# Kernel optimization log

Measured on AMD Instinct MI355X. Metric: run time of the kernel, lower is better.

Reference implementation:

```python
import jax, jax.numpy as jnp
import numpy as np

def setup_inputs() -> dict:
    key = jax.random.key(0)
    k1, k2, k3, k4 = jax.random.split(key, 4)
    B, S, IN, OUT = 4, 2048, 4096, 11008
    x = jax.random.normal(k1, (B, S, IN), dtype=jnp.float32)
    int8_weight = jax.random.randint(k2, (OUT, IN), -128, 128, dtype=jnp.int32)
    scale = jax.random.uniform(k3, (1,), dtype=jnp.float32) * 0.01 + 1e-4
    bias = jax.random.normal(k4, (OUT,), dtype=jnp.float32)
    return {"x": x, "int8_weight": int8_weight, "scale": scale, "bias": bias}

def reference(x, int8_weight, scale, bias):
    # dequantize int8 weight with per-tensor scale, then linear: y = x @ W^T + b
    weight = int8_weight.astype(jnp.float32) * scale[0]  # [OUT, IN]
    return jnp.einsum('bsi,oi->bso', x, weight) + bias
```

## Files before the change

kernel.cpp:

```cpp
#include <hip/hip_runtime.h>
#include <stdint.h>

typedef __attribute__((ext_vector_type(4))) int   int4v;
typedef __attribute__((ext_vector_type(4))) float f32x4;

#define K_DIM 4096
#define N_DIM 11008
#define M_DIM 8192
#define BM 256
#define BN 256
#define BKB 128
#define NT (K_DIM / BKB)
#define MT2 (M_DIM / BM)
#define NT2 (N_DIM / BN)

__global__ __launch_bounds__(256) void quant_x_kernel(
    const float* __restrict__ x, unsigned char* __restrict__ xq,
    float* __restrict__ srow)
{
    const int row = blockIdx.x;
    const float4* xr = (const float4*)(x + (size_t)row * K_DIM);
    float4 v[4];
    float m = 0.f;
    #pragma unroll
    for (int i = 0; i < 4; ++i) {
        v[i] = xr[threadIdx.x + 256 * i];
        m = fmaxf(m, fmaxf(fmaxf(fabsf(v[i].x), fabsf(v[i].y)),
                           fmaxf(fabsf(v[i].z), fabsf(v[i].w))));
    }
    #pragma unroll
    for (int off = 32; off; off >>= 1) m = fmaxf(m, __shfl_xor(m, off, 64));
    __shared__ float wmax[4];
    if ((threadIdx.x & 63) == 0) wmax[threadIdx.x >> 6] = m;
    __syncthreads();
    const float mb  = fmaxf(fmaxf(wmax[0], wmax[1]), fmaxf(wmax[2], wmax[3]));
    const float s   = (mb > 0.f) ? mb * (1.f / 127.f) : 1.f;
    const float inv = (mb > 0.f) ? 127.f / mb : 0.f;
    if (threadIdx.x == 0) srow[row] = s;
    uint32_t* oq = (uint32_t*)(xq + (size_t)row * K_DIM);
    #pragma unroll
    for (int i = 0; i < 4; ++i) {
        int a = __float2int_rn(v[i].x * inv), b = __float2int_rn(v[i].y * inv);
        int c = __float2int_rn(v[i].z * inv), d = __float2int_rn(v[i].w * inv);
        oq[threadIdx.x + 256 * i] =
            (a & 0xff) | ((b & 0xff) << 8) | ((c & 0xff) << 16) | ((d & 0xff) << 24);
    }
}

__global__ void cvt_w8_kernel(const int* __restrict__ w,
                              uint2* __restrict__ wq, int n8) {
    int i = blockIdx.x * blockDim.x + threadIdx.x;
    if (i >= n8) return;
    const int4* p = (const int4*)w + 2 * (size_t)i;
    int4 a = p[0], b = p[1];
    uint32_t lo = (a.x & 0xff) | ((a.y & 0xff) << 8) | ((a.z & 0xff) << 16) | ((a.w & 0xff) << 24);
    uint32_t hi = (b.x & 0xff) | ((b.y & 0xff) << 8) | ((b.z & 0xff) << 16) | ((b.w & 0xff) << 24);
    wq[i] = (uint2){lo, hi};
}

#define GLDS16(gsrc, ldst)                                                       \
    __builtin_amdgcn_global_load_lds(                                            \
        (const __attribute__((address_space(1))) void*)(gsrc),                   \
        (__attribute__((address_space(3))) void*)(ldst), 16, 0, 0)

#define BARSCHED() do { __builtin_amdgcn_s_barrier();                            \
                        __builtin_amdgcn_sched_barrier(0); } while (0)
#define VMCNT(n)  asm volatile("s_waitcnt vmcnt(" #n ")" ::: "memory")

__global__ __launch_bounds__(512, 2) void gemm2_kernel(
    const unsigned char* __restrict__ xq,
    const unsigned char* __restrict__ wq,
    const float* __restrict__ srow,
    const float* __restrict__ scale,
    const float* __restrict__ bias,
    float* __restrict__ out)
{
    __shared__ unsigned char sm[131072];
    char* smc = (char*)sm;

    const int T  = threadIdx.x;
    const int l  = T & 63;
    const int wv = T >> 6;
    const int wm = wv >> 2;
    const int wn = wv & 3;

    const int orig = blockIdx.x;
    const int xcd  = orig & 7;
    const int p    = orig >> 3;
    const int bm   = xcd * 4 + (p & 3);
    const int bn   = p >> 2;
    const size_t rowM0 = (size_t)bm * BM;
    const size_t rowN0 = (size_t)bn * BN;

    const int rowT = T >> 3;
    const int colT = (((T & 7) * 16) ^ ((rowT & 7) << 4));
    const unsigned char* pAg = xq + (rowM0 + rowT) * (size_t)K_DIM + colT;
    const unsigned char* pBg = wq + (rowN0 + ((rowT >> 5) << 6) + (rowT & 31)) * (size_t)K_DIM + colT;

    auto stageA = [&](char* base, int Q, int kt) {
        #pragma unroll
        for (int c = 0; c < 2; ++c) {
            const unsigned char* src = pAg + (size_t)(c * 128 + Q * 64) * K_DIM + (size_t)kt * BKB;
            char* dst = base + Q * 16384 + c * 8192 + T * 16;
            GLDS16(src, dst);
        }
    };
    auto stageB = [&](char* base, int Q, int kt) {
        #pragma unroll
        for (int c = 0; c < 2; ++c) {
            const unsigned char* src = pBg + (size_t)(c * 128 + Q * 32) * K_DIM + (size_t)kt * BKB;
            char* dst = base + 32768 + Q * 16384 + c * 8192 + T * 16;
            GLDS16(src, dst);
        }
    };

    const int sw     = (l & 7) << 4;
    const int inrow0 = (l >> 4) * 16;
    const int lowk0  = inrow0 ^ sw;
    const int lowk1  = (64 + inrow0) ^ sw;
    const int arow   = wm * 64 + (l & 15);
    const int brow   = wn * 32 + (l & 15);

    int4v acc[8][4];
    #pragma unroll
    for (int i = 0; i < 8; ++i)
        #pragma unroll
        for (int j = 0; j < 4; ++j)
            acc[i][j] = (int4v){0, 0, 0, 0};

    int4v Ah[4][2];
    int4v Bh[4][2];

    char* const b0 = smc;
    char* const b1 = smc + 65536;

#define READ_A(base)                                                             \
    _Pragma("unroll")                                                            \
    for (int im = 0; im < 4; ++im) {                                             \
        Ah[im][0] = *(const int4v*)((base) + (arow + im * 16) * 128 + lowk0);    \
        Ah[im][1] = *(const int4v*)((base) + (arow + im * 16) * 128 + lowk1);    \
    }
#define READ_B(base, f0)                                                         \
    _Pragma("unroll")                                                            \
    for (int f = 0; f < 2; ++f) {                                                \
        Bh[(f0) + f][0] = *(const int4v*)((base) + (brow + f * 16) * 128 + lowk0); \
        Bh[(f0) + f][1] = *(const int4v*)((base) + (brow + f * 16) * 128 + lowk1); \
    }
#define MFMAQ(mi, ni)                                                            \
    __builtin_amdgcn_s_setprio(1);                                               \
    _Pragma("unroll")                                                            \
    for (int im = 0; im < 4; ++im)                                               \
        _Pragma("unroll")                                                        \
        for (int jn = 0; jn < 2; ++jn)                                           \
            _Pragma("unroll")                                                    \
            for (int kk = 0; kk < 2; ++kk)                                       \
                acc[(mi) + im][(ni) + jn] = __builtin_amdgcn_mfma_i32_16x16x64_i8( \
                    Ah[im][kk], Bh[(ni) + jn][kk], acc[(mi) + im][(ni) + jn], 0, 0, 0); \
    __builtin_amdgcn_s_setprio(0);

#define TILE_BODY(bcur, bnxt, EE, ST0, STN, RD)                                  \
    READ_B((bcur) + 32768 + 16384, 2);                                           \
    if (ST0) stageA((bnxt), 1, (EE) + 1);                                        \
    BARSCHED();                                                                  \
    MFMAQ(0, 0);                                                                 \
    __builtin_amdgcn_sched_barrier(0);                                           \
    if (STN) stageA((bcur), 0, (EE) + 2);                                        \
    BARSCHED();                                                                  \
    MFMAQ(0, 2);                                                                 \
    READ_A((bcur) + 16384);                                                      \
    __builtin_amdgcn_sched_barrier(0);                                           \
    if (STN) stageB((bcur), 0, (EE) + 2);                                        \
    BARSCHED();                                                                  \
    MFMAQ(4, 0);                                                                 \
    if (STN) VMCNT(8); else VMCNT(4);                                            \
    __builtin_amdgcn_sched_barrier(0);                                           \
    if (STN) stageB((bcur), 1, (EE) + 2);                                        \
    BARSCHED();                                                                  \
    MFMAQ(4, 2);                                                                 \
    if (RD) { READ_A(bnxt); READ_B((bnxt) + 32768, 0); }                         \
    if (STN) VMCNT(6); else VMCNT(0);                                            \
    __builtin_amdgcn_s_barrier();                                                \
    __builtin_amdgcn_sched_barrier(0);

    stageA(b0, 0, 0); stageB(b0, 0, 0); stageB(b0, 1, 0); stageA(b0, 1, 0);
    stageA(b1, 0, 1); stageB(b1, 0, 1); stageB(b1, 1, 1);
    VMCNT(8);
    __builtin_amdgcn_s_barrier();
    __builtin_amdgcn_sched_barrier(0);
    READ_A(b0);
    READ_B(b0 + 32768, 0);
    VMCNT(6);
    __builtin_amdgcn_sched_barrier(0);

    for (int kt2 = 0; kt2 < NT / 2; ++kt2) {
        const int  E  = kt2 * 2;
        const bool st = (kt2 < NT / 2 - 1);
        TILE_BODY(b0, b1, E, true, st, true);
        TILE_BODY(b1, b0, E + 1, st, st, st);
    }

    const float s = scale[0];
    #pragma unroll
    for (int fm = 0; fm < 8; ++fm) {
        const size_t row0 = rowM0 + wm * 128 + fm * 16 + (l >> 4) * 4;
        const float4 sr4 = *(const float4*)(srow + row0);
        #pragma unroll
        for (int fn = 0; fn < 4; ++fn) {
            const int col = (int)rowN0 + wn * 64 + fn * 16 + (l & 15);
            const float bv = bias[col];
            float* o = out + row0 * N_DIM + col;
            o[0]                  = (float)acc[fm][fn][0] * (sr4.x * s) + bv;
            o[(size_t)1 * N_DIM]  = (float)acc[fm][fn][1] * (sr4.y * s) + bv;
            o[(size_t)2 * N_DIM]  = (float)acc[fm][fn][2] * (sr4.z * s) + bv;
            o[(size_t)3 * N_DIM]  = (float)acc[fm][fn][3] * (sr4.w * s) + bv;
        }
    }
}

extern "C" void kernel_launch(void* const* d_in, const int* in_sizes, int n_in,
                              void* d_out, int out_size, void* d_ws, size_t ws_size,
                              hipStream_t stream) {
    const float* x     = (const float*)d_in[0];
    const int*   w     = (const int*)d_in[1];
    const float* scale = (const float*)d_in[2];
    const float* bias  = (const float*)d_in[3];
    float*       out   = (float*)d_out;

    const size_t x_elems = (size_t)M_DIM * K_DIM;
    const size_t w_elems = (size_t)N_DIM * K_DIM;
    const size_t xq_off  = 0;
    const size_t wq_off  = x_elems;
    const size_t sr_off  = x_elems + w_elems;
    if (ws_size < sr_off + (size_t)M_DIM * 4) return;

    unsigned char* xqp = (unsigned char*)d_ws + xq_off;
    unsigned char* wqp = (unsigned char*)d_ws + wq_off;
    float*         srp = (float*)((unsigned char*)d_ws + sr_off);

    quant_x_kernel<<<M_DIM, 256, 0, stream>>>(x, xqp, srp);
    {
        int n8 = (int)(w_elems / 8);
        cvt_w8_kernel<<<(n8 + 255) / 256, 256, 0, stream>>>(w, (uint2*)wqp, n8);
    }
    gemm2_kernel<<<MT2 * NT2, 512, 0, stream>>>(xqp, wqp, srp, scale, bias, out);
}
```

Baseline: 432.2 us.

## Restructure int8 GEMM tile pipeline with explicit LDS waits and per-tile reads

Reworks the double-buffered main loop of the int8 MFMA GEMM. The first A/B fragment reads are moved from the tail of the previous tile into the start of each tile, explicit lgkmcnt waits and extra barriers are added around every MFMA quadrant, and all four stage loads for the next-next tile are issued within the current buffer's body. The aim is a simpler, more regular schedule with clearer LDS/global-load dependencies. The cost is less overlap between LDS reads and MFMAs, plus more barriers, which may stall the waves.

```diff
diff --git a/kernel.cpp b/kernel.cpp
--- a/kernel.cpp
+++ b/kernel.cpp
@@ -63,9 +63,11 @@
         (const __attribute__((address_space(1))) void*)(gsrc),                   \
         (__attribute__((address_space(3))) void*)(ldst), 16, 0, 0)
 
-#define BARSCHED() do { __builtin_amdgcn_s_barrier();                            \
-                        __builtin_amdgcn_sched_barrier(0); } while (0)
+#define SCHED0()  __builtin_amdgcn_sched_barrier(0)
+#define BARRIER() __builtin_amdgcn_s_barrier()
 #define VMCNT(n)  asm volatile("s_waitcnt vmcnt(" #n ")" ::: "memory")
+#define LGKM0()   do { asm volatile("s_waitcnt lgkmcnt(0)" ::: "memory"); SCHED0(); } while (0)
+#define LGKM8()   do { asm volatile("s_waitcnt lgkmcnt(8)" ::: "memory"); SCHED0(); } while (0)
 
 __global__ __launch_bounds__(512, 2) void gemm2_kernel(
     const unsigned char* __restrict__ xq,
@@ -158,45 +160,47 @@
                     Ah[im][kk], Bh[(ni) + jn][kk], acc[(mi) + im][(ni) + jn], 0, 0, 0); \
     __builtin_amdgcn_s_setprio(0);
 
-#define TILE_BODY(bcur, bnxt, EE, ST0, STN, RD)                                  \
+#define TILE_BODY(bcur, EE, STN)                                                 \
+                                                                         \
+    READ_A(bcur);                                                                \
+    READ_B((bcur) + 32768, 0);                                                   \
+    LGKM8();                                                                     \
+    BARRIER(); SCHED0();                                                         \
+    LGKM0();                                                                     \
+    MFMAQ(0, 0);                                                                 \
+    BARRIER(); SCHED0();                                                         \
+                                                                         \
     READ_B((bcur) + 32768 + 16384, 2);                                           \
-    if (ST0) stageA((bnxt), 1, (EE) + 1);                                        \
-    BARSCHED();                                                                  \
-    MFMAQ(0, 0);                                                                 \
-    __builtin_amdgcn_sched_barrier(0);                                           \
     if (STN) stageA((bcur), 0, (EE) + 2);                                        \
-    BARSCHED();                                                                  \
+    BARRIER(); SCHED0();                                                         \
+    LGKM0();                                                                     \
     MFMAQ(0, 2);                                                                 \
+    BARRIER(); SCHED0();                                                         \
+                                                                         \
     READ_A((bcur) + 16384);                                                      \
-    __builtin_amdgcn_sched_barrier(0);                                           \
     if (STN) stageB((bcur), 0, (EE) + 2);                                        \
-    BARSCHED();                                                                  \
+    BARRIER(); SCHED0();                                                         \
+    LGKM0();                                                                     \
     MFMAQ(4, 0);                                                                 \
-    if (STN) VMCNT(8); else VMCNT(4);                                            \
-    __builtin_amdgcn_sched_barrier(0);                                           \
-    if (STN) stageB((bcur), 1, (EE) + 2);                                        \
-    BARSCHED();                                                                  \
+    BARRIER(); SCHED0();                                                         \
+                                                                         \
+    if (STN) { stageB((bcur), 1, (EE) + 2); stageA((bcur), 1, (EE) + 2); }       \
+    BARRIER(); SCHED0();                                                         \
     MFMAQ(4, 2);                                                                 \
-    if (RD) { READ_A(bnxt); READ_B((bnxt) + 32768, 0); }                         \
-    if (STN) VMCNT(6); else VMCNT(0);                                            \
-    __builtin_amdgcn_s_barrier();                                                \
-    __builtin_amdgcn_sched_barrier(0);
+    if (STN) VMCNT(8); else VMCNT(0);                                            \
+    BARRIER(); SCHED0();
 
     stageA(b0, 0, 0); stageB(b0, 0, 0); stageB(b0, 1, 0); stageA(b0, 1, 0);
-    stageA(b1, 0, 1); stageB(b1, 0, 1); stageB(b1, 1, 1);
+    stageA(b1, 0, 1); stageB(b1, 0, 1); stageB(b1, 1, 1); stageA(b1, 1, 1);
     VMCNT(8);
-    __builtin_amdgcn_s_barrier();
-    __builtin_amdgcn_sched_barrier(0);
-    READ_A(b0);
-    READ_B(b0 + 32768, 0);
-    VMCNT(6);
-    __builtin_amdgcn_sched_barrier(0);
+    BARRIER(); SCHED0();
 
     for (int kt2 = 0; kt2 < NT / 2; ++kt2) {
-        const int  E  = kt2 * 2;
-        const bool st = (kt2 < NT / 2 - 1);
-        TILE_BODY(b0, b1, E, true, st, true);
-        TILE_BODY(b1, b0, E + 1, st, st, st);
+        const int  E   = kt2 * 2;
+        const bool st0 = (E + 2 < NT);
+        const bool st1 = (E + 3 < NT);
+        TILE_BODY(b0, E,     st0);
+        TILE_BODY(b1, E + 1, st1);
     }
 
     const float s = scale[0];
```

Result: slower. 452.6 us (+4.7%).
